# Kernel optimization log

Measured on AMD Instinct MI355X. Metric: run time of the kernel, lower is better.

Reference implementation:

```python
import jax, jax.numpy as jnp
import numpy as np

B, D, H, W = 16, 512, 64, 64
K = 64  # clusters
EPS = 1e-12  # torch F.normalize eps


def _l2norm(v, axis):
    n = jnp.linalg.norm(v, axis=axis, keepdims=True)
    return v / jnp.maximum(n, EPS)


def setup_inputs() -> dict:
    key = jax.random.key(0)
    k1, k2, k3, k4 = jax.random.split(key, 4)
    x = jax.random.normal(k1, (B, D, H, W), dtype=jnp.float32)
    # conv weight/bias are independent trainable params after init; sample them
    centers = jax.random.uniform(k2, (K, D), dtype=jnp.float32)
    conv_w = 2.0 * 100.0 * centers + 0.01 * jax.random.normal(k3, (K, D), dtype=jnp.float32)
    conv_b = -100.0 * jnp.linalg.norm(centers, axis=1) + 0.01 * jax.random.normal(k4, (K,), dtype=jnp.float32)
    return {"x": x, "conv_w": conv_w, "conv_b": conv_b, "centers": centers}


def reference(x, conv_w, conv_b, centers):
    b = x.shape[0]
    x_flat = x.reshape(b, D, -1)                       # (B, D, N)
    # 1x1 conv == per-location linear over channels
    logits = jnp.einsum('bdn,kd->bkn', x_flat, conv_w) + conv_b[None, :, None]
    w = jax.nn.softmax(logits, axis=1)                 # softmax over clusters
    # vlad[b,k,d] = sum_n w[b,k,n]*(x[b,d,n] - c[k,d])
    #            = (w @ x^T)[b,k,d] - (sum_n w[b,k,n]) * c[k,d]
    wx = jnp.einsum('bkn,bdn->bkd', w, x_flat)         # (B, K, D)
    wsum = jnp.sum(w, axis=-1)                          # (B, K)
    vlad = wx - wsum[:, :, None] * centers[None]        # (B, K, D)
    vlad = _l2norm(vlad, axis=2)                        # intra-normalize
    vlad = vlad.reshape(b, -1)
    vlad = _l2norm(vlad, axis=1)                        # global L2
    return vlad
```

## Files before the change

### kernel.cpp

```cpp
#include <hip/hip_runtime.h>
#include <hip/hip_bf16.h>
#include <math.h>

#define B_ 16
#define D_ 512
#define N_ 4096
#define K_ 64

typedef __attribute__((ext_vector_type(8))) short bfrag;
typedef __attribute__((ext_vector_type(4))) float f32x4;

static __device__ __forceinline__ float bf2f(unsigned short u) {
    return __uint_as_float(((unsigned)u) << 16);
}
static __device__ __forceinline__ unsigned short f2bf(float v) {
    __hip_bfloat16 h = __float2bfloat16(v);
    union { __hip_bfloat16 h; unsigned short u; } cv; cv.h = h; return cv.u;
}
static __device__ __forceinline__ void split3(float v, unsigned short& h,
                                              unsigned short& m, unsigned short& l) {
    h = f2bf(v); float r1 = v - bf2f(h);
    m = f2bf(r1); float r2 = r1 - bf2f(m);
    l = f2bf(r2);
}
static __device__ __forceinline__ void split2(float v, unsigned short& h,
                                              unsigned short& l) {
    h = f2bf(v); l = f2bf(v - bf2f(h));
}
#define MFMA(a, b, c) __builtin_amdgcn_mfma_f32_16x16x32_bf16((a), (b), (c), 0, 0, 0)

__global__ __launch_bounds__(256) void k_prep(
    const float* __restrict__ conv_w, unsigned short* __restrict__ cwL)
{
    const int i = blockIdx.x * 256 + threadIdx.x;
    const float4 v = *(const float4*)&conv_w[i * 4];
    const float vv[4] = {v.x, v.y, v.z, v.w};
    unsigned short h[4], m[4], l[4];
    #pragma unroll
    for (int j = 0; j < 4; ++j) split3(vv[j], h[j], m[j], l[j]);
    *(ushort4*)&cwL[0 * (K_ * D_) + i * 4] = make_ushort4(h[0], h[1], h[2], h[3]);
    *(ushort4*)&cwL[1 * (K_ * D_) + i * 4] = make_ushort4(m[0], m[1], m[2], m[3]);
    *(ushort4*)&cwL[2 * (K_ * D_) + i * 4] = make_ushort4(l[0], l[1], l[2], l[3]);
}

__global__ __launch_bounds__(256, 5) void k_logits_softmax(
    const float* __restrict__ x, const unsigned short* __restrict__ cwL,
    const float* __restrict__ conv_b,
    unsigned int* __restrict__ whl, float* __restrict__ wsumbuf)
{
    const int b   = blockIdx.x >> 5;
    const int n0  = (blockIdx.x & 31) * 128;
    const int tid  = threadIdx.x;
    const int w    = tid >> 6;
    const int lane = tid & 63;
    const int q = lane >> 4;
    const int c = lane & 15;
    const int ktb = (w & 1) * 32;
    const int ntb = (w >> 1) * 64;

    __shared__ unsigned short xs[3][128][40];
    __shared__ float redm[2][128];
    __shared__ float reds[2][128];

    f32x4 acc[2][4];
    #pragma unroll
    for (int kt = 0; kt < 2; ++kt)
        #pragma unroll
        for (int nt = 0; nt < 4; ++nt) acc[kt][nt] = (f32x4){0.f, 0.f, 0.f, 0.f};

    const float* xb = x + (size_t)b * D_ * N_ + n0;
    const unsigned short* cwp = cwL + (ktb + c) * D_ + q * 8;

    for (int d0 = 0; d0 < D_; d0 += 32) {
        bfrag af[2][3];
        #pragma unroll
        for (int kt = 0; kt < 2; ++kt)
            #pragma unroll
            for (int lv = 0; lv < 3; ++lv)
                af[kt][lv] = *(const bfrag*)(cwp + lv * (K_ * D_) + kt * 16 * D_ + d0);
        #pragma unroll
        for (int i = 0; i < 4; ++i) {
            const int s  = i * 256 + tid;
            const int xn = s & 127;
            const int j  = s >> 7;
            const int Cs = ((j >> 1) ^ ((xn >> 3) & 3));
            const int dsw = (Cs * 2 + (j & 1)) * 4;
            const int dg4 = j * 4;
            unsigned short h[4], m[4], l[4];
            #pragma unroll
            for (int r = 0; r < 4; ++r) {
                const float v = xb[(size_t)(d0 + dg4 + r) * N_ + xn];
                split3(v, h[r], m[r], l[r]);
            }
            *(ushort4*)&xs[0][xn][dsw] = make_ushort4(h[0], h[1], h[2], h[3]);
            *(ushort4*)&xs[1][xn][dsw] = make_ushort4(m[0], m[1], m[2], m[3]);
            *(ushort4*)&xs[2][xn][dsw] = make_ushort4(l[0], l[1], l[2], l[3]);
        }
        __syncthreads();

        #pragma unroll
        for (int nt = 0; nt < 4; ++nt) {
            const int row = ntb + nt * 16 + c;
            const int qs  = (q ^ ((row >> 3) & 3)) * 8;
            bfrag bf[3];
            #pragma unroll
            for (int lv = 0; lv < 3; ++lv)
                bf[lv] = *(const bfrag*)&xs[lv][row][qs];
            #pragma unroll
            for (int kt = 0; kt < 2; ++kt) {
                f32x4 a = acc[kt][nt];
                a = MFMA(af[kt][0], bf[0], a);
                a = MFMA(af[kt][0], bf[1], a);
                a = MFMA(af[kt][1], bf[0], a);
                a = MFMA(af[kt][1], bf[1], a);
                a = MFMA(af[kt][0], bf[2], a);
                a = MFMA(af[kt][2], bf[0], a);
                acc[kt][nt] = a;
            }
        }
        __syncthreads();
    }

    #pragma unroll
    for (int kt = 0; kt < 2; ++kt)
        #pragma unroll
        for (int r = 0; r < 4; ++r) {
            const float bias = conv_b[ktb + kt * 16 + q * 4 + r];
            #pragma unroll
            for (int nt = 0; nt < 4; ++nt) acc[kt][nt][r] += bias;
        }

    float mloc[4];
    #pragma unroll
    for (int nt = 0; nt < 4; ++nt) {
        float m = acc[0][nt][0];
        #pragma unroll
        for (int kt = 0; kt < 2; ++kt)
            #pragma unroll
            for (int r = 0; r < 4; ++r) m = fmaxf(m, acc[kt][nt][r]);
        m = fmaxf(m, __shfl_xor(m, 16));
        m = fmaxf(m, __shfl_xor(m, 32));
        mloc[nt] = m;
    }
    if (q == 0)
        #pragma unroll
        for (int nt = 0; nt < 4; ++nt) redm[w & 1][ntb + nt * 16 + c] = mloc[nt];
    __syncthreads();
    float mall[4];
    #pragma unroll
    for (int nt = 0; nt < 4; ++nt)
        mall[nt] = fmaxf(redm[0][ntb + nt * 16 + c], redm[1][ntb + nt * 16 + c]);

    float sloc[4] = {0.f, 0.f, 0.f, 0.f};
    #pragma unroll
    for (int nt = 0; nt < 4; ++nt) {
        #pragma unroll
        for (int kt = 0; kt < 2; ++kt)
            #pragma unroll
            for (int r = 0; r < 4; ++r) {
                const float e = __expf(acc[kt][nt][r] - mall[nt]);
                acc[kt][nt][r] = e;
                sloc[nt] += e;
            }
        sloc[nt] += __shfl_xor(sloc[nt], 16);
        sloc[nt] += __shfl_xor(sloc[nt], 32);
    }
    if (q == 0)
        #pragma unroll
        for (int nt = 0; nt < 4; ++nt) reds[w & 1][ntb + nt * 16 + c] = sloc[nt];
    __syncthreads();

    float wacc[2][4] = {{0.f, 0.f, 0.f, 0.f}, {0.f, 0.f, 0.f, 0.f}};
    #pragma unroll
    for (int nt = 0; nt < 4; ++nt) {
        const float inv = 1.0f / (reds[0][ntb + nt * 16 + c] + reds[1][ntb + nt * 16 + c]);
        #pragma unroll
        for (int kt = 0; kt < 2; ++kt)
            #pragma unroll
            for (int r = 0; r < 4; ++r) {
                const float v = acc[kt][nt][r] * inv;
                unsigned short hi, lo;
                split2(v, hi, lo);
                const size_t idx = ((size_t)b * K_ + ktb + kt * 16 + q * 4 + r) * N_
                                 + n0 + ntb + nt * 16 + c;
                whl[idx] = (unsigned)hi | ((unsigned)lo << 16);
                wacc[kt][r] += v;
            }
    }
    #pragma unroll
    for (int msk = 1; msk < 16; msk <<= 1)
        #pragma unroll
        for (int kt = 0; kt < 2; ++kt)
            #pragma unroll
            for (int r = 0; r < 4; ++r)
                wacc[kt][r] += __shfl_xor(wacc[kt][r], msk);
    if (c == 0)
        #pragma unroll
        for (int kt = 0; kt < 2; ++kt)
            #pragma unroll
            for (int r = 0; r < 4; ++r)
                atomicAdd(&wsumbuf[b * K_ + ktb + kt * 16 + q * 4 + r], wacc[kt][r]);
}

__global__ __launch_bounds__(256, 5) void k_wx(
    const float* __restrict__ x, const unsigned int* __restrict__ whl,
    float* __restrict__ vlad)
{
    const int nc = blockIdx.x & 7;
    const int dc = (blockIdx.x >> 3) & 3;
    const int b  = blockIdx.x >> 5;
    const int tid  = threadIdx.x;
    const int w    = tid >> 6;
    const int lane = tid & 63;
    const int q = lane >> 4;
    const int c = lane & 15;
    const int ktb = (w & 1) * 32;
    const int dtb = (w >> 1) * 64;

    __shared__ unsigned short ws2[2][64][40];
    __shared__ unsigned short xs2[2][128][40];

    f32x4 acc[2][4];
    #pragma unroll
    for (int kt = 0; kt < 2; ++kt)
        #pragma unroll
        for (int dt = 0; dt < 4; ++dt) acc[kt][dt] = (f32x4){0.f, 0.f, 0.f, 0.f};

    const float* xb = x + (size_t)b * D_ * N_ + (size_t)dc * 128 * N_;
    const unsigned int* wb = whl + (size_t)b * K_ * N_;

    const int wk = tid >> 2;
    const int wn = (tid & 3) * 8;
    const int xd = tid >> 3;
    const int xn = (tid & 7) * 4;

    const int nbase = nc * 512;
    for (int n0 = nbase; n0 < nbase + 512; n0 += 32) {
        {
            const uint4 a = *(const uint4*)&wb[(size_t)wk * N_ + n0 + wn];
            const uint4 bq = *(const uint4*)&wb[(size_t)wk * N_ + n0 + wn + 4];
            bfrag h8, l8;
            h8[0] = (short)(unsigned short)a.x;  l8[0] = (short)(unsigned short)(a.x >> 16);
            h8[1] = (short)(unsigned short)a.y;  l8[1] = (short)(unsigned short)(a.y >> 16);
            h8[2] = (short)(unsigned short)a.z;  l8[2] = (short)(unsigned short)(a.z >> 16);
            h8[3] = (short)(unsigned short)a.w;  l8[3] = (short)(unsigned short)(a.w >> 16);
            h8[4] = (short)(unsigned short)bq.x; l8[4] = (short)(unsigned short)(bq.x >> 16);
            h8[5] = (short)(unsigned short)bq.y; l8[5] = (short)(unsigned short)(bq.y >> 16);
            h8[6] = (short)(unsigned short)bq.z; l8[6] = (short)(unsigned short)(bq.z >> 16);
            h8[7] = (short)(unsigned short)bq.w; l8[7] = (short)(unsigned short)(bq.w >> 16);
            *(bfrag*)&ws2[0][wk][wn] = h8;
            *(bfrag*)&ws2[1][wk][wn] = l8;
        }
        #pragma unroll
        for (int i = 0; i < 4; ++i) {
            const float4 v = *(const float4*)&xb[(size_t)(i * 32 + xd) * N_ + n0 + xn];
            const float vv[4] = {v.x, v.y, v.z, v.w};
            unsigned short h[4], l[4];
            #pragma unroll
            for (int j = 0; j < 4; ++j) split2(vv[j], h[j], l[j]);
            *(ushort4*)&xs2[0][i * 32 + xd][xn] = make_ushort4(h[0], h[1], h[2], h[3]);
            *(ushort4*)&xs2[1][i * 32 + xd][xn] = make_ushort4(l[0], l[1], l[2], l[3]);
        }
        __syncthreads();

        bfrag afh[2], afl[2];
        #pragma unroll
        for (int kt = 0; kt < 2; ++kt) {
            afh[kt] = *(const bfrag*)&ws2[0][ktb + kt * 16 + c][q * 8];
            afl[kt] = *(const bfrag*)&ws2[1][ktb + kt * 16 + c][q * 8];
        }
        #pragma unroll
        for (int dt = 0; dt < 4; ++dt) {
            const bfrag bh = *(const bfrag*)&xs2[0][dtb + dt * 16 + c][q * 8];
            const bfrag bl = *(const bfrag*)&xs2[1][dtb + dt * 16 + c][q * 8];
            #pragma unroll
            for (int kt = 0; kt < 2; ++kt) {
                f32x4 a = acc[kt][dt];
                a = MFMA(afh[kt], bh, a);
                a = MFMA(afh[kt], bl, a);
                a = MFMA(afl[kt], bh, a);
                acc[kt][dt] = a;
            }
        }
        __syncthreads();
    }

    #pragma unroll
    for (int kt = 0; kt < 2; ++kt)
        #pragma unroll
        for (int dt = 0; dt < 4; ++dt)
            #pragma unroll
            for (int r = 0; r < 4; ++r) {
                const int k = ktb + kt * 16 + q * 4 + r;
                const int d = dc * 128 + dtb + dt * 16 + c;
                atomicAdd(&vlad[((size_t)b * K_ + k) * D_ + d], acc[kt][dt][r]);
            }
}

__global__ __launch_bounds__(256) void k_norm(
    const float* __restrict__ wsumbuf, const float* __restrict__ vlad,
    const float* __restrict__ centers, float* __restrict__ out)
{
    const int b = blockIdx.x >> 6;
    const int k = blockIdx.x & 63;
    const int tid = threadIdx.x;

    const float wsum = wsumbuf[b * K_ + k];

    const float* vr = vlad + ((size_t)b * K_ + k) * D_;
    const float* cr = centers + k * D_;
    const float v0 = vr[tid]       - wsum * cr[tid];
    const float v1 = vr[tid + 256] - wsum * cr[tid + 256];

    float ss = v0 * v0 + v1 * v1;
    __shared__ float red2[4];
    #pragma unroll
    for (int off = 32; off > 0; off >>= 1) ss += __shfl_down(ss, off, 64);
    if ((tid & 63) == 0) red2[tid >> 6] = ss;
    __syncthreads();
    const float nrm = sqrtf(red2[0] + red2[1] + red2[2] + red2[3]);
    const float scale = 1.0f / (8.0f * fmaxf(nrm, 1e-12f));

    float* outr = out + ((size_t)b * K_ + k) * D_;
    outr[tid]       = v0 * scale;
    outr[tid + 256] = v1 * scale;
}

extern "C" void kernel_launch(void* const* d_in, const int* in_sizes, int n_in,
                              void* d_out, int out_size, void* d_ws, size_t ws_size,
                              hipStream_t stream) {
    const float* x       = (const float*)d_in[0];
    const float* conv_w  = (const float*)d_in[1];
    const float* conv_b  = (const float*)d_in[2];
    const float* centers = (const float*)d_in[3];
    float* out = (float*)d_out;

    char* wsb = (char*)d_ws;
    float* vlad         = (float*)wsb;
    float* wsumbuf      = (float*)(wsb + (2u << 20));
    unsigned int* whl   = (unsigned int*)(wsb + (3u << 20));
    unsigned short* cwL = (unsigned short*)(wsb + (20u << 20));

    hipMemsetAsync(vlad, 0, (2u << 20) + 4096, stream);

    k_prep<<<32, 256, 0, stream>>>(conv_w, cwL);
    k_logits_softmax<<<B_ * 32, 256, 0, stream>>>(x, cwL, conv_b, whl, wsumbuf);
    k_wx<<<B_ * 4 * 8, 256, 0, stream>>>(x, whl, vlad);
    k_norm<<<B_ * K_, 256, 0, stream>>>(wsumbuf, vlad, centers, out);
}
```

Before: 256.9 us.

## Double-buffer x staging and prefetch weights in logits kernel

Restructures the logits/softmax kernel main loop into a software pipeline: LDS tiles are double-buffered and the global loads of the next x slice and conv-weight fragments are issued into registers before computing the current slice. This is meant to hide global-memory latency behind the MFMA work and removes one barrier per step. It doubles the LDS footprint and raises register pressure, and the occupancy hint of 5 blocks per CU is dropped from both the logits kernel and the wx kernel, which may lower occupancy.

Measured after the change: 244.9 us. 1.05x faster.

```diff
diff --git a/kernel.cpp b/kernel.cpp
--- a/kernel.cpp
+++ b/kernel.cpp
@@ -43,7 +43,7 @@
     *(ushort4*)&cwL[2 * (K_ * D_) + i * 4] = make_ushort4(l[0], l[1], l[2], l[3]);
 }
 
-__global__ __launch_bounds__(256, 5) void k_logits_softmax(
+__global__ __launch_bounds__(256) void k_logits_softmax(
     const float* __restrict__ x, const unsigned short* __restrict__ cwL,
     const float* __restrict__ conv_b,
     unsigned int* __restrict__ whl, float* __restrict__ wsumbuf)
@@ -58,7 +58,7 @@
     const int ktb = (w & 1) * 32;
     const int ntb = (w >> 1) * 64;
 
-    __shared__ unsigned short xs[3][128][40];
+    __shared__ unsigned short xs[2][3][128][40];
     __shared__ float redm[2][128];
     __shared__ float reds[2][128];
 
@@ -71,33 +71,43 @@
     const float* xb = x + (size_t)b * D_ * N_ + n0;
     const unsigned short* cwp = cwL + (ktb + c) * D_ + q * 8;
 
-    for (int d0 = 0; d0 < D_; d0 += 32) {
-        bfrag af[2][3];
+    const int xn = tid & 127;
+    const int jh = tid >> 7;
+
+    float gx[4][4];
+    bfrag afA[2][3], afB[2][3];
+
+    auto LOADX = [&](int d0) {
+        #pragma unroll
+        for (int i = 0; i < 4; ++i) {
+            const int dg4 = 8 * i + jh * 4;
+            #pragma unroll
+            for (int r = 0; r < 4; ++r)
+                gx[i][r] = xb[(size_t)(d0 + dg4 + r) * N_ + xn];
+        }
+    };
+    auto LOADAF = [&](bfrag (&af)[2][3], int d0) {
         #pragma unroll
         for (int kt = 0; kt < 2; ++kt)
             #pragma unroll
             for (int lv = 0; lv < 3; ++lv)
                 af[kt][lv] = *(const bfrag*)(cwp + lv * (K_ * D_) + kt * 16 * D_ + d0);
+    };
+    auto STAGE = [&](int buf) {
         #pragma unroll
         for (int i = 0; i < 4; ++i) {
-            const int s  = i * 256 + tid;
-            const int xn = s & 127;
-            const int j  = s >> 7;
-            const int Cs = ((j >> 1) ^ ((xn >> 3) & 3));
+            const int j   = 2 * i + jh;
+            const int Cs  = i ^ ((xn >> 3) & 3);
             const int dsw = (Cs * 2 + (j & 1)) * 4;
-            const int dg4 = j * 4;
             unsigned short h[4], m[4], l[4];
             #pragma unroll
-            for (int r = 0; r < 4; ++r) {
-                const float v = xb[(size_t)(d0 + dg4 + r) * N_ + xn];
-                split3(v, h[r], m[r], l[r]);
-            }
-            *(ushort4*)&xs[0][xn][dsw] = make_ushort4(h[0], h[1], h[2], h[3]);
-            *(ushort4*)&xs[1][xn][dsw] = make_ushort4(m[0], m[1], m[2], m[3]);
-            *(ushort4*)&xs[2][xn][dsw] = make_ushort4(l[0], l[1], l[2], l[3]);
-        }
-        __syncthreads();
-
+            for (int r = 0; r < 4; ++r) split3(gx[i][r], h[r], m[r], l[r]);
+            *(ushort4*)&xs[buf][0][xn][dsw] = make_ushort4(h[0], h[1], h[2], h[3]);
+            *(ushort4*)&xs[buf][1][xn][dsw] = make_ushort4(m[0], m[1], m[2], m[3]);
+            *(ushort4*)&xs[buf][2][xn][dsw] = make_ushort4(l[0], l[1], l[2], l[3]);
+        }
+    };
+    auto COMPUTE = [&](int buf, bfrag (&af)[2][3]) {
         #pragma unroll
         for (int nt = 0; nt < 4; ++nt) {
             const int row = ntb + nt * 16 + c;
@@ -105,7 +115,7 @@
             bfrag bf[3];
             #pragma unroll
             for (int lv = 0; lv < 3; ++lv)
-                bf[lv] = *(const bfrag*)&xs[lv][row][qs];
+                bf[lv] = *(const bfrag*)&xs[buf][lv][row][qs];
             #pragma unroll
             for (int kt = 0; kt < 2; ++kt) {
                 f32x4 a = acc[kt][nt];
@@ -118,7 +128,28 @@
                 acc[kt][nt] = a;
             }
         }
+    };
+
+    LOADX(0);
+    LOADAF(afA, 0);
+    STAGE(0);
+    LOADX(32);
+    LOADAF(afB, 32);
+    __syncthreads();
+
+    #pragma unroll 1
+    for (int tt = 0; tt < 8; ++tt) {
+        const int de = tt * 64;
+        COMPUTE(0, afA);
+        STAGE(1);
+        if (de + 64 < D_) { LOADX(de + 64); LOADAF(afA, de + 64); }
         __syncthreads();
+        COMPUTE(1, afB);
+        if (de + 64 < D_) {
+            STAGE(0);
+            if (de + 96 < D_) { LOADX(de + 96); LOADAF(afB, de + 96); }
+            __syncthreads();
+        }
     }
 
     #pragma unroll
@@ -202,7 +233,7 @@
                 atomicAdd(&wsumbuf[b * K_ + ktb + kt * 16 + q * 4 + r], wacc[kt][r]);
 }
 
-__global__ __launch_bounds__(256, 5) void k_wx(
+__global__ __launch_bounds__(256) void k_wx(
     const float* __restrict__ x, const unsigned int* __restrict__ whl,
     float* __restrict__ vlad)
 {
@@ -237,7 +268,7 @@
     const int nbase = nc * 512;
     for (int n0 = nbase; n0 < nbase + 512; n0 += 32) {
         {
-            const uint4 a = *(const uint4*)&wb[(size_t)wk * N_ + n0 + wn];
+            const uint4 a  = *(const uint4*)&wb[(size_t)wk * N_ + n0 + wn];
             const uint4 bq = *(const uint4*)&wb[(size_t)wk * N_ + n0 + wn + 4];
             bfrag h8, l8;
             h8[0] = (short)(unsigned short)a.x;  l8[0] = (short)(unsigned short)(a.x >> 16);
```
